# Kernel tuning notes

Hardware: AMD Instinct MI355X
Metric: run time of the kernel (lower is better)

## Reference

```python
import jax, jax.numpy as jnp
import numpy as np

N = 200_000   # nodes
E = 3_200_000 # edges (avg degree 16)
H = 64        # hidden_size == state_size
A = 2         # annotation_size


def _mlp(x, w1, b1, w2, b2, w3, b3):
    x = jax.nn.relu(x @ w1.T + b1)
    x = jax.nn.relu(x @ w2.T + b2)
    return x @ w3.T + b3


def setup_inputs() -> dict:
    key = jax.random.key(0)
    ks = jax.random.split(key, 24)
    s = 0.1
    d = {}
    d["x0"] = jax.random.normal(ks[0], (N, H - A), jnp.float32)
    d["annotations"] = jax.random.uniform(ks[1], (N, A), jnp.float32)
    d["edges"] = jax.random.randint(ks[2], (E, 2), 0, N, jnp.int32)
    d["eligible"] = jax.random.randint(ks[3], (4096,), 0, N, jnp.int32)
    d["W_msg"] = jax.random.normal(ks[4], (H, H), jnp.float32) * s
    d["b_msg"] = jnp.zeros((H,), jnp.float32)
    d["gru_Wih"] = jax.random.normal(ks[5], (3 * H, H), jnp.float32) * s
    d["gru_Whh"] = jax.random.normal(ks[6], (3 * H, H), jnp.float32) * s
    d["gru_bih"] = jnp.zeros((3 * H,), jnp.float32)
    d["gru_bhh"] = jnp.zeros((3 * H,), jnp.float32)
    # MLP heads: (prefix, out_dim)
    heads = [("sn", 1), ("st", 2), ("co", 128), ("sp", 100)]
    i = 7
    for p, od in heads:
        d[p + "_w1"] = jax.random.normal(ks[i], (64, H), jnp.float32) * s; i += 1
        d[p + "_b1"] = jnp.zeros((64,), jnp.float32)
        d[p + "_w2"] = jax.random.normal(ks[i], (64, 64), jnp.float32) * s; i += 1
        d[p + "_w2"] = d[p + "_w2"]
        d[p + "_b2"] = jnp.zeros((64,), jnp.float32)
        d[p + "_w3"] = jax.random.normal(ks[i], (od, 64), jnp.float32) * s; i += 1
        d[p + "_b3"] = jnp.zeros((od,), jnp.float32)
    return d


def _ggnn(x0, annotations, edges, W_msg, b_msg, gru_Wih, gru_Whh, gru_bih, gru_bhh):
    # initial node state: annotations appended, padded to hidden_size  -> [N, H]
    h = jnp.concatenate([x0, annotations], axis=-1)
    src, dst = edges[:, 0], edges[:, 1]
    # one edge type, one timestep (layer_timesteps=[1])
    m = h[src] @ W_msg.T + b_msg                       # [E, H] gather + tiny GEMM
    agg = jax.ops.segment_sum(m, dst, num_segments=h.shape[0])  # [N, H] scatter-add
    # torch.nn.GRUCell(agg, h); gate order: r, z, n
    gx = agg @ gru_Wih.T + gru_bih
    gh = h @ gru_Whh.T + gru_bhh
    xr, xz, xn = jnp.split(gx, 3, axis=-1)
    hr, hz, hn = jnp.split(gh, 3, axis=-1)
    r = jax.nn.sigmoid(xr + hr)
    z = jax.nn.sigmoid(xz + hz)
    n = jnp.tanh(xn + r * hn)
    return (1.0 - z) * n + z * h


def reference(x0, annotations, edges, eligible, W_msg, b_msg, gru_Wih, gru_Whh,
              gru_bih, gru_bhh, sn_w1, sn_b1, sn_w2, sn_b2, sn_w3, sn_b3,
              st_w1, st_b1, st_w2, st_b2, st_w3, st_b3,
              co_w1, co_b1, co_w2, co_b2, co_w3, co_b3,
              sp_w1, sp_b1, sp_w2, sp_b2, sp_w3, sp_b3):
    h = _ggnn(x0, annotations, edges, W_msg, b_msg, gru_Wih, gru_Whh, gru_bih, gru_bhh)
    select_out = _mlp(h, sn_w1, sn_b1, sn_w2, sn_b2, sn_w3, sn_b3)  # [N, 1]
    rel = jnp.argmax(select_out[eligible, 0])
    node_index = eligible[rel]
    h_node = h[node_index]                                           # [H]
    task_out = _mlp(h_node, st_w1, st_b1, st_w2, st_b2, st_w3, st_b3)   # [2]
    color_out = _mlp(h_node, co_w1, co_b1, co_w2, co_b2, co_w3, co_b3)  # [128]
    split_out = _mlp(h_node, sp_w1, sp_b1, sp_w2, sp_b2, sp_w3, sp_b3)  # [100]
    return (select_out, node_index, task_out, color_out, split_out)
```

## Files before the change

kernel.cpp:

```cpp
#include <hip/hip_runtime.h>

#define THREADS 256
#define CAP 10240

__device__ __forceinline__ float sigm_(float x) {
  return 1.0f / (1.0f + __expf(-x));
}
__device__ __forceinline__ float tanh_(float x) {
  float cx = fminf(15.0f, fmaxf(-15.0f, x));
  float a = __expf(2.0f * cx);
  return (a - 1.0f) / (a + 1.0f);
}

__global__ void k_build_h(const float* __restrict__ x0, const float* __restrict__ ann,
                          float* __restrict__ h, int N) {
  int t = blockIdx.x * THREADS + threadIdx.x;
  if (t >= N * 64) return;
  int v = t >> 6, c = t & 63;
  h[t] = (c < 62) ? x0[v * 62 + c] : ann[(v << 1) + (c - 62)];
}

__global__ void k_pre(const float* __restrict__ Wmsg, const float* __restrict__ bmsg,
                      const float* __restrict__ Wih, const float* __restrict__ Whh,
                      const float* __restrict__ sw1, const float* __restrict__ sw2,
                      float* __restrict__ Wct, float* __restrict__ Whht,
                      float* __restrict__ bmc, float* __restrict__ w1t, float* __restrict__ w2t) {
  int g = blockIdx.x * THREADS + threadIdx.x;
  int gs = gridDim.x * THREADS;
  for (int idx = g; idx < 64 * 192; idx += gs) {
    int k = idx / 192, r = idx - k * 192;
    float acc = 0.f;
    for (int c = 0; c < 64; ++c) acc = fmaf(Wih[r * 64 + c], Wmsg[c * 64 + k], acc);
    Wct[idx]  = acc;
    Whht[idx] = Whh[r * 64 + k];
  }
  for (int r = g; r < 192; r += gs) {
    float acc = 0.f;
    for (int c = 0; c < 64; ++c) acc = fmaf(Wih[r * 64 + c], bmsg[c], acc);
    bmc[r] = acc;
  }
  for (int idx = g; idx < 64 * 64; idx += gs) {
    int k = idx >> 6, r = idx & 63;
    w1t[idx] = sw1[r * 64 + k];
    w2t[idx] = sw2[r * 64 + k];
  }
}


__global__ __launch_bounds__(THREADS) void k_binA(const int* __restrict__ edges,
                                                  int* __restrict__ bincnt,
                                                  int* __restrict__ binbuf, int E, int nbins) {
  __shared__ int cnt[1024];
  __shared__ int gb[1024];
  int t = threadIdx.x;
  for (int i = t; i < nbins; i += THREADS) cnt[i] = 0;
  __syncthreads();
  long e0 = (long)blockIdx.x * 2048;
  int bins[8], packs[8], ranks[8];
#pragma unroll
  for (int j = 0; j < 8; ++j) {
    long e = e0 + j * THREADS + t;
    bins[j] = -1;
    if (e < E) {
      int2 ed = ((const int2*)edges)[e];
      bins[j] = ed.y >> 9;
      packs[j] = (ed.x << 9) | (ed.y & 511);
      ranks[j] = atomicAdd(&cnt[bins[j]], 1);
    }
  }
  __syncthreads();
  for (int i = t; i < nbins; i += THREADS) gb[i] = cnt[i] ? atomicAdd(&bincnt[i], cnt[i]) : 0;
  __syncthreads();
#pragma unroll
  for (int j = 0; j < 8; ++j)
    if (bins[j] >= 0) {
      int pos = gb[bins[j]] + ranks[j];
      if (pos < CAP) binbuf[(long)bins[j] * CAP + pos] = packs[j];
    }
}

__global__ void k_binscan(const int* __restrict__ bincnt, int* __restrict__ binoff,
                          int* __restrict__ row_off, int nbins, int E, int N) {
  __shared__ int sm[1024];
  int t = threadIdx.x;
  sm[t] = (t < nbins) ? bincnt[t] : 0;
  __syncthreads();
  for (int o = 1; o < 1024; o <<= 1) {
    int v = (t >= o) ? sm[t - o] : 0;
    __syncthreads();
    sm[t] += v;
    __syncthreads();
  }
  if (t < nbins) binoff[t] = (t == 0) ? 0 : sm[t - 1];
  if (t == 0) { binoff[nbins] = E; row_off[N] = E; }
}

__global__ __launch_bounds__(THREADS) void k_binB(const int* __restrict__ binoff,
                                                  const int* __restrict__ bincnt,
                                                  const int* __restrict__ binbuf,
                                                  int* __restrict__ csr,
                                                  int* __restrict__ deg,
                                                  int* __restrict__ row_off, int N) {
  __shared__ int cnt[512], off[512], cur[512], ps[THREADS];
  int b = blockIdx.x, t = threadIdx.x;
  int nodebase = b << 9;
  int nn = min(512, N - nodebase);
  int ebeg = binoff[b];
  int cntE = min(bincnt[b], CAP);
  const int* seg = binbuf + (long)b * CAP;
  for (int i = t; i < 512; i += THREADS) cnt[i] = 0;
  __syncthreads();
  for (int e = t; e < cntE; e += THREADS)
    atomicAdd(&cnt[seg[e] & 511], 1);
  __syncthreads();
  int a0 = cnt[2 * t], a1 = cnt[2 * t + 1];
  ps[t] = a0 + a1;
  __syncthreads();
  for (int o = 1; o < THREADS; o <<= 1) {
    int v = (t >= o) ? ps[t - o] : 0;
    __syncthreads();
    ps[t] += v;
    __syncthreads();
  }
  int excl = (t == 0) ? 0 : ps[t - 1];
  off[2 * t] = excl;          cur[2 * t] = excl;
  off[2 * t + 1] = excl + a0; cur[2 * t + 1] = excl + a0;
  __syncthreads();
  for (int l = t; l < nn; l += THREADS) {
    deg[nodebase + l] = cnt[l];
    row_off[nodebase + l] = ebeg + off[l];
  }
  for (int e = t; e < cntE; e += THREADS) {
    int p = seg[e];
    int slot = atomicAdd(&cur[p & 511], 1);
    csr[ebeg + slot] = p >> 9;
  }
}

__global__ __launch_bounds__(THREADS, 3) void k_gru_sel(
    const int* __restrict__ row_off, const int* __restrict__ csr,
    const float* __restrict__ h, float* __restrict__ hn,
    const float* __restrict__ Wct, const float* __restrict__ Whht,
    const float* __restrict__ bmc, const float* __restrict__ bih, const float* __restrict__ bhh,
    const int* __restrict__ deg,
    const float* __restrict__ w1t, const float* __restrict__ b1,
    const float* __restrict__ w2t, const float* __restrict__ b2,
    const float* __restrict__ w3, const float* __restrict__ b3,
    float* __restrict__ sel_out) {
  __shared__ float St[64][68];
  __shared__ float Ht[64][68];
  const int t = threadIdx.x;
  const long base = (long)blockIdx.x * (64 * 64);
  const int nodebase = blockIdx.x * 64;

#pragma unroll
  for (int j = 0; j < 4; ++j) {
    int f = t + THREADS * j;
    int n = f >> 4;
    int k0 = (f & 15) << 2;
    float4 hv = *(const float4*)(h + base + n * 64 + k0);
    Ht[k0 + 0][n] = hv.x; Ht[k0 + 1][n] = hv.y; Ht[k0 + 2][n] = hv.z; Ht[k0 + 3][n] = hv.w;
  }

  {
    const float SC = 1048576.0f;
    const float ISC = 1.0f / 1048576.0f;
    int vl = t >> 2;
    int c16 = (t & 3) << 4;
    int v = nodebase + vl;
    int beg = row_off[v], end = row_off[v + 1];
    int acc[16];
#pragma unroll
    for (int j = 0; j < 16; ++j) acc[j] = 0;
    for (int i = beg; i < end; ++i) {
      const float4* hp = (const float4*)(h + (long)csr[i] * 64 + c16);
      float4 a = hp[0], b = hp[1], c = hp[2], d = hp[3];
      acc[0]  += __float2int_rn(a.x * SC); acc[1]  += __float2int_rn(a.y * SC);
      acc[2]  += __float2int_rn(a.z * SC); acc[3]  += __float2int_rn(a.w * SC);
      acc[4]  += __float2int_rn(b.x * SC); acc[5]  += __float2int_rn(b.y * SC);
      acc[6]  += __float2int_rn(b.z * SC); acc[7]  += __float2int_rn(b.w * SC);
      acc[8]  += __float2int_rn(c.x * SC); acc[9]  += __float2int_rn(c.y * SC);
      acc[10] += __float2int_rn(c.z * SC); acc[11] += __float2int_rn(c.w * SC);
      acc[12] += __float2int_rn(d.x * SC); acc[13] += __float2int_rn(d.y * SC);
      acc[14] += __float2int_rn(d.z * SC); acc[15] += __float2int_rn(d.w * SC);
    }
#pragma unroll
    for (int j = 0; j < 16; ++j) St[c16 + j][vl] = (float)acc[j] * ISC;
  }
  __syncthreads();

  const int ng = t & 15, rg = t >> 4;
  const int n4 = ng << 2, c0 = rg << 2;

  float arz[2][4][4] = {};
  float axn[4][4] = {};
  float ahn[4][4] = {};

  for (int k = 0; k < 64; ++k) {
    const float4 s4 = *(const float4*)&St[k][n4];
    const float4 h4 = *(const float4*)&Ht[k][n4];
    const float sv[4] = {s4.x, s4.y, s4.z, s4.w};
    const float hv[4] = {h4.x, h4.y, h4.z, h4.w};
    const float* wxp = Wct + k * 192 + c0;
    const float* whp = Whht + k * 192 + c0;
#pragma unroll
    for (int sec = 0; sec < 2; ++sec) {
      const float4 wx = *(const float4*)(wxp + sec * 64);
      const float4 wh = *(const float4*)(whp + sec * 64);
      const float wxv[4] = {wx.x, wx.y, wx.z, wx.w};
      const float whv[4] = {wh.x, wh.y, wh.z, wh.w};
#pragma unroll
      for (int ci = 0; ci < 4; ++ci)
#pragma unroll
        for (int nj = 0; nj < 4; ++nj) {
          arz[sec][ci][nj] = fmaf(wxv[ci], sv[nj], arz[sec][ci][nj]);
          arz[sec][ci][nj] = fmaf(whv[ci], hv[nj], arz[sec][ci][nj]);
        }
    }
    {
      const float4 wx = *(const float4*)(wxp + 128);
      const float4 wh = *(const float4*)(whp + 128);
      const float wxv[4] = {wx.x, wx.y, wx.z, wx.w};
      const float whv[4] = {wh.x, wh.y, wh.z, wh.w};
#pragma unroll
      for (int ci = 0; ci < 4; ++ci)
#pragma unroll
        for (int nj = 0; nj < 4; ++nj) {
          axn[ci][nj] = fmaf(wxv[ci], sv[nj], axn[ci][nj]);
          ahn[ci][nj] = fmaf(whv[ci], hv[nj], ahn[ci][nj]);
        }
    }
  }

  float degf[4];
#pragma unroll
  for (int nj = 0; nj < 4; ++nj) degf[nj] = (float)deg[nodebase + n4 + nj];

  float res[4][4];
#pragma unroll
  for (int ci = 0; ci < 4; ++ci) {
    const int c = c0 + ci;
    const float br = bmc[c];       const float cr = bih[c] + bhh[c];
    const float bz = bmc[64 + c];  const float cz = bih[64 + c] + bhh[64 + c];
    const float bn = bmc[128 + c]; const float ci2 = bih[128 + c];
    const float ch = bhh[128 + c];
#pragma unroll
    for (int nj = 0; nj < 4; ++nj) {
      float r = sigm_(arz[0][ci][nj] + degf[nj] * br + cr);
      float z = sigm_(arz[1][ci][nj] + degf[nj] * bz + cz);
      float xn = axn[ci][nj] + degf[nj] * bn + ci2;
      float hnv = ahn[ci][nj] + ch;
      float nn = tanh_(fmaf(r, hnv, xn));
      float hold = Ht[c][n4 + nj];
      res[ci][nj] = fmaf(1.f - z, nn, z * hold);
    }
  }
#pragma unroll
  for (int nj = 0; nj < 4; ++nj) {
    float4 o = make_float4(res[0][nj], res[1][nj], res[2][nj], res[3][nj]);
    *(float4*)(hn + base + (n4 + nj) * 64 + c0) = o;
  }

  __syncthreads();
#pragma unroll
  for (int ci = 0; ci < 4; ++ci) {
    *(float4*)&St[c0 + ci][n4] = make_float4(res[ci][0], res[ci][1], res[ci][2], res[ci][3]);
  }
  __syncthreads();

  float acc[4][4] = {};
  for (int k = 0; k < 64; ++k) {
    const float4 a4 = *(const float4*)&St[k][n4];
    const float av[4] = {a4.x, a4.y, a4.z, a4.w};
    const float4 w4 = *(const float4*)(w1t + k * 64 + c0);
    const float wv[4] = {w4.x, w4.y, w4.z, w4.w};
#pragma unroll
    for (int ri = 0; ri < 4; ++ri)
#pragma unroll
      for (int nj = 0; nj < 4; ++nj)
        acc[ri][nj] = fmaf(wv[ri], av[nj], acc[ri][nj]);
  }
  __syncthreads();
#pragma unroll
  for (int ri = 0; ri < 4; ++ri) {
    const float bb = b1[c0 + ri];
    float4 o;
    o.x = fmaxf(acc[ri][0] + bb, 0.f);
    o.y = fmaxf(acc[ri][1] + bb, 0.f);
    o.z = fmaxf(acc[ri][2] + bb, 0.f);
    o.w = fmaxf(acc[ri][3] + bb, 0.f);
    *(float4*)&Ht[c0 + ri][n4] = o;
  }
  __syncthreads();

  float acc2[4][4] = {};
  for (int k = 0; k < 64; ++k) {
    const float4 a4 = *(const float4*)&Ht[k][n4];
    const float av[4] = {a4.x, a4.y, a4.z, a4.w};
    const float4 w4 = *(const float4*)(w2t + k * 64 + c0);
    const float wv[4] = {w4.x, w4.y, w4.z, w4.w};
#pragma unroll
    for (int ri = 0; ri < 4; ++ri)
#pragma unroll
      for (int nj = 0; nj < 4; ++nj)
        acc2[ri][nj] = fmaf(wv[ri], av[nj], acc2[ri][nj]);
  }
  __syncthreads();
#pragma unroll
  for (int ri = 0; ri < 4; ++ri) {
    const float bb = b2[c0 + ri];
    float4 o;
    o.x = fmaxf(acc2[ri][0] + bb, 0.f);
    o.y = fmaxf(acc2[ri][1] + bb, 0.f);
    o.z = fmaxf(acc2[ri][2] + bb, 0.f);
    o.w = fmaxf(acc2[ri][3] + bb, 0.f);
    *(float4*)&St[c0 + ri][n4] = o;
  }
  __syncthreads();

  if (t < 64) {
    float acc3 = b3[0];
    for (int k = 0; k < 64; ++k) acc3 = fmaf(St[k][t], w3[k], acc3);
    sel_out[nodebase + t] = acc3;
  }
}

__global__ void k_argmax(const float* __restrict__ sel, const int* __restrict__ elig,
                         int ne, float* __restrict__ out_idx, int* __restrict__ idx_ws) {
  __shared__ float bv[256];
  __shared__ int br[256];
  const int t = threadIdx.x;
  float best = -3.402823466e+38f;
  int brel = 0x7fffffff;
  for (int i = t; i < ne; i += 256) {
    float v = sel[elig[i]];
    if (v > best || (v == best && i < brel)) { best = v; brel = i; }
  }
  bv[t] = best; br[t] = brel;
  __syncthreads();
  for (int off = 128; off > 0; off >>= 1) {
    if (t < off) {
      float v2 = bv[t + off]; int r2 = br[t + off];
      if (v2 > bv[t] || (v2 == bv[t] && r2 < br[t])) { bv[t] = v2; br[t] = r2; }
    }
    __syncthreads();
  }
  if (t == 0) {
    int node = elig[br[0]];
    out_idx[0] = (float)node;
    idx_ws[0] = node;
  }
}

struct HeadP {
  const float *w1, *b1, *w2, *b2, *w3, *b3;
  int od, off;
};

__global__ void k_heads(const float* __restrict__ hnew, const int* __restrict__ idx_p,
                        HeadP p0, HeadP p1, HeadP p2, float* __restrict__ outF) {
  HeadP p = (blockIdx.x == 0) ? p0 : ((blockIdx.x == 1) ? p1 : p2);
  __shared__ float hh[64], a1[64], a2[64];
  const int t = threadIdx.x;
  const int node = idx_p[0];
  if (t < 64) hh[t] = hnew[(long)node * 64 + t];
  __syncthreads();
  if (t < 64) {
    float acc = p.b1[t];
    for (int k = 0; k < 64; ++k) acc = fmaf(p.w1[t * 64 + k], hh[k], acc);
    a1[t] = fmaxf(acc, 0.f);
  }
  __syncthreads();
  if (t < 64) {
    float acc = p.b2[t];
    for (int k = 0; k < 64; ++k) acc = fmaf(p.w2[t * 64 + k], a1[k], acc);
    a2[t] = fmaxf(acc, 0.f);
  }
  __syncthreads();
  for (int o = t; o < p.od; o += blockDim.x) {
    float acc = p.b3[o];
    for (int k = 0; k < 64; ++k) acc = fmaf(p.w3[o * 64 + k], a2[k], acc);
    outF[p.off + o] = acc;
  }
}

extern "C" void kernel_launch(void* const* d_in, const int* in_sizes, int n_in,
                              void* d_out, int out_size, void* d_ws, size_t ws_size,
                              hipStream_t stream) {
  const float* x0    = (const float*)d_in[0];
  const float* ann   = (const float*)d_in[1];
  const int*   edges = (const int*)d_in[2];
  const int*   elig  = (const int*)d_in[3];
  const float* Wmsg  = (const float*)d_in[4];
  const float* bmsg  = (const float*)d_in[5];
  const float* Wih   = (const float*)d_in[6];
  const float* Whh   = (const float*)d_in[7];
  const float* bih   = (const float*)d_in[8];
  const float* bhh   = (const float*)d_in[9];

  const int N  = in_sizes[0] / 62;
  const int E  = in_sizes[2] / 2;
  const int NE = in_sizes[3];
  const int NBINS = (N + 511) >> 9;

  float* ws = (float*)d_ws;
  size_t off = 0;
  float* hn      = ws + off; off += (size_t)N * 64;
  int*   deg     = (int*)(ws + off); off += N;
  float* h       = ws + off; off += (size_t)N * 64;
  float* Wct     = ws + off; off += 64 * 192;
  float* Whht    = ws + off; off += 64 * 192;
  float* bmc     = ws + off; off += 192;
  float* w1t     = ws + off; off += 64 * 64;
  float* w2t     = ws + off; off += 64 * 64;
  int*   idxp    = (int*)(ws + off); off += 1;
  int*   row_off = (int*)(ws + off); off += (size_t)N + 1;
  int*   bincnt  = (int*)(ws + off); off += 1024;
  int*   binoff  = (int*)(ws + off); off += 1025;
  int*   csr     = (int*)(ws + off); off += E;
  int*   binbuf  = (int*)hn;

  float* outF = (float*)d_out;

  hipMemsetAsync(bincnt, 0, 1024 * sizeof(int), stream);

  k_build_h<<<(N * 64 + THREADS - 1) / THREADS, THREADS, 0, stream>>>(x0, ann, h, N);
  k_pre<<<64, THREADS, 0, stream>>>(Wmsg, bmsg, Wih, Whh,
                                    (const float*)d_in[10], (const float*)d_in[12],
                                    Wct, Whht, bmc, w1t, w2t);

  const int EB = (E + 2047) / 2048;
  k_binA<<<EB, THREADS, 0, stream>>>(edges, bincnt, binbuf, E, NBINS);
  k_binscan<<<1, 1024, 0, stream>>>(bincnt, binoff, row_off, NBINS, E, N);
  k_binB<<<NBINS, THREADS, 0, stream>>>(binoff, bincnt, binbuf, csr, deg, row_off, N);

  k_gru_sel<<<N / 64, THREADS, 0, stream>>>(row_off, csr, h, hn,
                                            Wct, Whht, bmc, bih, bhh, deg,
                                            w1t, (const float*)d_in[11],
                                            w2t, (const float*)d_in[13],
                                            (const float*)d_in[14], (const float*)d_in[15],
                                            outF);
  k_argmax<<<1, 256, 0, stream>>>(outF, elig, NE, outF + N, idxp);

  HeadP p0 = {(const float*)d_in[16], (const float*)d_in[17], (const float*)d_in[18],
              (const float*)d_in[19], (const float*)d_in[20], (const float*)d_in[21],
              2, N + 1};
  HeadP p1 = {(const float*)d_in[22], (const float*)d_in[23], (const float*)d_in[24],
              (const float*)d_in[25], (const float*)d_in[26], (const float*)d_in[27],
              128, N + 3};
  HeadP p2 = {(const float*)d_in[28], (const float*)d_in[29], (const float*)d_in[30],
              (const float*)d_in[31], (const float*)d_in[32], (const float*)d_in[33],
              100, N + 131};
  k_heads<<<3, 128, 0, stream>>>(hn, idxp, p0, p1, p2, outF);
}
```

Baseline: 628.4 us.

## Drop CSR build; sort bin edges per block in LDS inside GRU kernel

Removes the binscan and binB kernels. Each GRU block now scans its 512-node bin buffer, keeps edges for its own 64 nodes, and builds a local CSR in shared memory, which it uses for the gather. It also fuses build_h with the weight precompute and argmax with the heads, which cuts launches. The trade-off is that each bin is read redundantly by eight blocks, plus more shared memory, and a risk of truncation if a 64-node group exceeds LCAP edges.

```diff
diff --git a/kernel.cpp b/kernel.cpp
--- a/kernel.cpp
+++ b/kernel.cpp
@@ -2,6 +2,7 @@
 
 #define THREADS 256
 #define CAP 10240
+#define LCAP 1408
 
 __device__ __forceinline__ float sigm_(float x) {
   return 1.0f / (1.0f + __expf(-x));
@@ -12,21 +13,23 @@
   return (a - 1.0f) / (a + 1.0f);
 }
 
-__global__ void k_build_h(const float* __restrict__ x0, const float* __restrict__ ann,
-                          float* __restrict__ h, int N) {
-  int t = blockIdx.x * THREADS + threadIdx.x;
-  if (t >= N * 64) return;
-  int v = t >> 6, c = t & 63;
-  h[t] = (c < 62) ? x0[v * 62 + c] : ann[(v << 1) + (c - 62)];
-}
-
-__global__ void k_pre(const float* __restrict__ Wmsg, const float* __restrict__ bmsg,
-                      const float* __restrict__ Wih, const float* __restrict__ Whh,
-                      const float* __restrict__ sw1, const float* __restrict__ sw2,
-                      float* __restrict__ Wct, float* __restrict__ Whht,
-                      float* __restrict__ bmc, float* __restrict__ w1t, float* __restrict__ w2t) {
-  int g = blockIdx.x * THREADS + threadIdx.x;
-  int gs = gridDim.x * THREADS;
+__global__ void k_init(const float* __restrict__ x0, const float* __restrict__ ann,
+                       float* __restrict__ h, int N, int NBH,
+                       const float* __restrict__ Wmsg, const float* __restrict__ bmsg,
+                       const float* __restrict__ Wih, const float* __restrict__ Whh,
+                       const float* __restrict__ sw1, const float* __restrict__ sw2,
+                       float* __restrict__ Wct, float* __restrict__ Whht,
+                       float* __restrict__ bmc, float* __restrict__ w1t,
+                       float* __restrict__ w2t) {
+  if (blockIdx.x < NBH) {
+    int t = blockIdx.x * THREADS + threadIdx.x;
+    if (t >= N * 64) return;
+    int v = t >> 6, c = t & 63;
+    h[t] = (c < 62) ? x0[v * 62 + c] : ann[(v << 1) + (c - 62)];
+    return;
+  }
+  int g = (blockIdx.x - NBH) * THREADS + threadIdx.x;
+  int gs = 64 * THREADS;
   for (int idx = g; idx < 64 * 192; idx += gs) {
     int k = idx / 192, r = idx - k * 192;
     float acc = 0.f;
@@ -45,7 +48,6 @@
     w2t[idx] = sw2[r * 64 + k];
   }
 }
-
 
 __global__ __launch_bounds__(THREADS) void k_binA(const int* __restrict__ edges,
                                                   int* __restrict__ bincnt,
@@ -79,79 +81,28 @@
     }
 }
 
-__global__ void k_binscan(const int* __restrict__ bincnt, int* __restrict__ binoff,
-                          int* __restrict__ row_off, int nbins, int E, int N) {
-  __shared__ int sm[1024];
-  int t = threadIdx.x;
-  sm[t] = (t < nbins) ? bincnt[t] : 0;
-  __syncthreads();
-  for (int o = 1; o < 1024; o <<= 1) {
-    int v = (t >= o) ? sm[t - o] : 0;
-    __syncthreads();
-    sm[t] += v;
-    __syncthreads();
-  }
-  if (t < nbins) binoff[t] = (t == 0) ? 0 : sm[t - 1];
-  if (t == 0) { binoff[nbins] = E; row_off[N] = E; }
-}
-
-__global__ __launch_bounds__(THREADS) void k_binB(const int* __restrict__ binoff,
-                                                  const int* __restrict__ bincnt,
-                                                  const int* __restrict__ binbuf,
-                                                  int* __restrict__ csr,
-                                                  int* __restrict__ deg,
-                                                  int* __restrict__ row_off, int N) {
-  __shared__ int cnt[512], off[512], cur[512], ps[THREADS];
-  int b = blockIdx.x, t = threadIdx.x;
-  int nodebase = b << 9;
-  int nn = min(512, N - nodebase);
-  int ebeg = binoff[b];
-  int cntE = min(bincnt[b], CAP);
-  const int* seg = binbuf + (long)b * CAP;
-  for (int i = t; i < 512; i += THREADS) cnt[i] = 0;
-  __syncthreads();
-  for (int e = t; e < cntE; e += THREADS)
-    atomicAdd(&cnt[seg[e] & 511], 1);
-  __syncthreads();
-  int a0 = cnt[2 * t], a1 = cnt[2 * t + 1];
-  ps[t] = a0 + a1;
-  __syncthreads();
-  for (int o = 1; o < THREADS; o <<= 1) {
-    int v = (t >= o) ? ps[t - o] : 0;
-    __syncthreads();
-    ps[t] += v;
-    __syncthreads();
-  }
-  int excl = (t == 0) ? 0 : ps[t - 1];
-  off[2 * t] = excl;          cur[2 * t] = excl;
-  off[2 * t + 1] = excl + a0; cur[2 * t + 1] = excl + a0;
-  __syncthreads();
-  for (int l = t; l < nn; l += THREADS) {
-    deg[nodebase + l] = cnt[l];
-    row_off[nodebase + l] = ebeg + off[l];
-  }
-  for (int e = t; e < cntE; e += THREADS) {
-    int p = seg[e];
-    int slot = atomicAdd(&cur[p & 511], 1);
-    csr[ebeg + slot] = p >> 9;
-  }
-}
-
 __global__ __launch_bounds__(THREADS, 3) void k_gru_sel(
-    const int* __restrict__ row_off, const int* __restrict__ csr,
+    const int* __restrict__ bincnt, const int* __restrict__ binbuf,
     const float* __restrict__ h, float* __restrict__ hn,
     const float* __restrict__ Wct, const float* __restrict__ Whht,
     const float* __restrict__ bmc, const float* __restrict__ bih, const float* __restrict__ bhh,
-    const int* __restrict__ deg,
     const float* __restrict__ w1t, const float* __restrict__ b1,
     const float* __restrict__ w2t, const float* __restrict__ b2,
     const float* __restrict__ w3, const float* __restrict__ b3,
     float* __restrict__ sel_out) {
   __shared__ float St[64][68];
   __shared__ float Ht[64][68];
+  __shared__ int elist[LCAP];
+  __shared__ int ecnt[64], eoff[64], ecur[64];
   const int t = threadIdx.x;
   const long base = (long)blockIdx.x * (64 * 64);
   const int nodebase = blockIdx.x * 64;
+  const int b512 = blockIdx.x >> 3;
+  const int sub = blockIdx.x & 7;
+  const int segn = min(bincnt[b512], CAP);
+  const int* seg = binbuf + (long)b512 * CAP;
+
+  if (t < 64) ecnt[t] = 0;
 
 #pragma unroll
   for (int j = 0; j < 4; ++j) {
@@ -161,19 +112,68 @@
     float4 hv = *(const float4*)(h + base + n * 64 + k0);
     Ht[k0 + 0][n] = hv.x; Ht[k0 + 1][n] = hv.y; Ht[k0 + 2][n] = hv.z; Ht[k0 + 3][n] = hv.w;
   }
+  __syncthreads();
+
+  for (int i = t; i < segn; i += THREADS) {
+    int p = seg[i];
+    if (((p >> 6) & 7) == sub) atomicAdd(&ecnt[p & 63], 1);
+  }
+  __syncthreads();
+  if (t < 64) eoff[t] = ecnt[t];
+  __syncthreads();
+  for (int o = 1; o < 64; o <<= 1) {
+    int v = (t >= o && t < 64) ? eoff[t - o] : 0;
+    __syncthreads();
+    if (t < 64) eoff[t] += v;
+    __syncthreads();
+  }
+  if (t < 64) { int ex = eoff[t] - ecnt[t]; eoff[t] = ex; ecur[t] = ex; }
+  __syncthreads();
+  for (int i = t; i < segn; i += THREADS) {
+    int p = seg[i];
+    if (((p >> 6) & 7) == sub) {
+      int slot = atomicAdd(&ecur[p & 63], 1);
+      if (slot < LCAP) elist[slot] = p >> 9;
+    }
+  }
+  __syncthreads();
 
   {
     const float SC = 1048576.0f;
     const float ISC = 1.0f / 1048576.0f;
     int vl = t >> 2;
     int c16 = (t & 3) << 4;
-    int v = nodebase + vl;
-    int beg = row_off[v], end = row_off[v + 1];
+    int beg = eoff[vl];
+    int num = min(ecnt[vl], LCAP - beg);
+    if (num < 0) num = 0;
     int acc[16];
 #pragma unroll
     for (int j = 0; j < 16; ++j) acc[j] = 0;
-    for (int i = beg; i < end; ++i) {
-      const float4* hp = (const float4*)(h + (long)csr[i] * 64 + c16);
+    int i = 0;
+    for (; i + 1 < num; i += 2) {
+      const float4* hp0 = (const float4*)(h + (long)elist[beg + i] * 64 + c16);
+      const float4* hp1 = (const float4*)(h + (long)elist[beg + i + 1] * 64 + c16);
+      float4 a0 = hp0[0], b0 = hp0[1], c0_ = hp0[2], d0 = hp0[3];
+      float4 a1 = hp1[0], b1_ = hp1[1], c1 = hp1[2], d1 = hp1[3];
+      acc[0]  += __float2int_rn(a0.x * SC) + __float2int_rn(a1.x * SC);
+      acc[1]  += __float2int_rn(a0.y * SC) + __float2int_rn(a1.y * SC);
+      acc[2]  += __float2int_rn(a0.z * SC) + __float2int_rn(a1.z * SC);
+      acc[3]  += __float2int_rn(a0.w * SC) + __float2int_rn(a1.w * SC);
+      acc[4]  += __float2int_rn(b0.x * SC) + __float2int_rn(b1_.x * SC);
+      acc[5]  += __float2int_rn(b0.y * SC) + __float2int_rn(b1_.y * SC);
+      acc[6]  += __float2int_rn(b0.z * SC) + __float2int_rn(b1_.z * SC);
+      acc[7]  += __float2int_rn(b0.w * SC) + __float2int_rn(b1_.w * SC);
+      acc[8]  += __float2int_rn(c0_.x * SC) + __float2int_rn(c1.x * SC);
+      acc[9]  += __float2int_rn(c0_.y * SC) + __float2int_rn(c1.y * SC);
+      acc[10] += __float2int_rn(c0_.z * SC) + __float2int_rn(c1.z * SC);
+      acc[11] += __float2int_rn(c0_.w * SC) + __float2int_rn(c1.w * SC);
+      acc[12] += __float2int_rn(d0.x * SC) + __float2int_rn(d1.x * SC);
+      acc[13] += __float2int_rn(d0.y * SC) + __float2int_rn(d1.y * SC);
+      acc[14] += __float2int_rn(d0.z * SC) + __float2int_rn(d1.z * SC);
+      acc[15] += __float2int_rn(d0.w * SC) + __float2int_rn(d1.w * SC);
+    }
+    if (i < num) {
+      const float4* hp = (const float4*)(h + (long)elist[beg + i] * 64 + c16);
       float4 a = hp[0], b = hp[1], c = hp[2], d = hp[3];
       acc[0]  += __float2int_rn(a.x * SC); acc[1]  += __float2int_rn(a.y * SC);
       acc[2]  += __float2int_rn(a.z * SC); acc[3]  += __float2int_rn(a.w * SC);
@@ -234,7 +234,7 @@
 
   float degf[4];
 #pragma unroll
-  for (int nj = 0; nj < 4; ++nj) degf[nj] = (float)deg[nodebase + n4 + nj];
+  for (int nj = 0; nj < 4; ++nj) degf[nj] = (float)ecnt[n4 + nj];
 
   float res[4][4];
 #pragma unroll
@@ -325,10 +325,18 @@
   }
 }
 
-__global__ void k_argmax(const float* __restrict__ sel, const int* __restrict__ elig,
-                         int ne, float* __restrict__ out_idx, int* __restrict__ idx_ws) {
+struct HeadP {
+  const float *w1, *b1, *w2, *b2, *w3, *b3;
+  int od, off;
+};
+
+__global__ void k_argmax_heads(const float* __restrict__ sel, const int* __restrict__ elig,
+                               int ne, const float* __restrict__ hnew,
+                               HeadP p0, HeadP p1, HeadP p2,
+                               float* __restrict__ outF, int N) {
   __shared__ float bv[256];
   __shared__ int br[256];
+  __shared__ float hh[64], a1[64], a2[64];
   const int t = threadIdx.x;
   float best = -3.402823466e+38f;
   int brel = 0x7fffffff;
@@ -347,40 +355,34 @@
   }
   if (t == 0) {
     int node = elig[br[0]];
-    out_idx[0] = (float)node;
-    idx_ws[0] = node;
-  }
-}
-
-struct HeadP {
-  const float *w1, *b1, *w2, *b2, *w3, *b3;
-  int od, off;
-};
-
-__global__ void k_heads(const float* __restrict__ hnew, const int* __restrict__ idx_p,
-                        HeadP p0, HeadP p1, HeadP p2, float* __restrict__ outF) {
-  HeadP p = (blockIdx.x == 0) ? p0 : ((blockIdx.x == 1) ? p1 : p2);
-  __shared__ float hh[64], a1[64], a2[64];
-  const int t = threadIdx.x;
-  const int node = idx_p[0];
+    outF[N] = (float)node;
+    br[0] = node;
+  }
+  __syncthreads();
+  const int node = br[0];
   if (t < 64) hh[t] = hnew[(long)node * 64 + t];
   __syncthreads();
-  if (t < 64) {
-    float acc = p.b1[t];
-    for (int k = 0; k < 64; ++k) acc = fmaf(p.w1[t * 64 + k], hh[k], acc);
-    a1[t] = fmaxf(acc, 0.f);
-  }
-  __syncthreads();
-  if (t < 64) {
-    float acc = p.b2[t];
-    for (int k = 0; k < 64; ++k) acc = fmaf(p.w2[t * 64 + k], a1[k], acc);
-    a2[t] = fmaxf(acc, 0.f);
-  }
-  __syncthreads();
-  for (int o = t; o < p.od; o += blockDim.x) {
-    float acc = p.b3[o];
-    for (int k = 0; k < 64; ++k) acc = fmaf(p.w3[o * 64 + k], a2[k], acc);
-    outF[p.off + o] = acc;
+
+  for (int hsel = 0; hsel < 3; ++hsel) {
+    HeadP p = (hsel == 0) ? p0 : ((hsel == 1) ? p1 : p2);
+    if (t < 64) {
+      float acc = p.b1[t];
+      for (int k = 0; k < 64; ++k) acc = fmaf(p.w1[t * 64 + k], hh[k], acc);
+      a1[t] = fmaxf(acc, 0.f);
+    }
+    __syncthreads();
+    if (t < 64) {
+      float acc = p.b2[t];
+      for (int k = 0; k < 64; ++k) acc = fmaf(p.w2[t * 64 + k], a1[k], acc);
+      a2[t] = fmaxf(acc, 0.f);
+    }
+    __syncthreads();
+    for (int o = t; o < p.od; o += 256) {
+      float acc = p.b3[o];
+      for (int k = 0; k < 64; ++k) acc = fmaf(p.w3[o * 64 + k], a2[k], acc);
+      outF[p.off + o] = acc;
+    }
+    __syncthreads();
   }
 }
 
@@ -406,41 +408,34 @@
   float* ws = (float*)d_ws;
   size_t off = 0;
   float* hn      = ws + off; off += (size_t)N * 64;
-  int*   deg     = (int*)(ws + off); off += N;
   float* h       = ws + off; off += (size_t)N * 64;
   float* Wct     = ws + off; off += 64 * 192;
   float* Whht    = ws + off; off += 64 * 192;
   float* bmc     = ws + off; off += 192;
   float* w1t     = ws + off; off += 64 * 64;
   float* w2t     = ws + off; off += 64 * 64;
-  int*   idxp    = (int*)(ws + off); off += 1;
-  int*   row_off = (int*)(ws + off); off += (size_t)N + 1;
   int*   bincnt  = (int*)(ws + off); off += 1024;
-  int*   binoff  = (int*)(ws + off); off += 1025;
-  int*   csr     = (int*)(ws + off); off += E;
-  int*   binbuf  = (int*)hn;
+  int*   binbuf  = (int*)(ws + off); off += (size_t)NBINS * CAP;
 
   float* outF = (float*)d_out;
 
   hipMemsetAsync(bincnt, 0, 1024 * sizeof(int), stream);
 
-  k_build_h<<<(N * 64 + THREADS - 1) / THREADS, THREADS, 0, stream>>>(x0, ann, h, N);
-  k_pre<<<64, THREADS, 0, stream>>>(Wmsg, bmsg, Wih, Whh,
-                                    (const float*)d_in[10], (const float*)d_in[12],
-                                    Wct, Whht, bmc, w1t, w2t);
+  const int NBH = (N * 64 + THREADS - 1) / THREADS;
+  k_init<<<NBH + 64, THREADS, 0, stream>>>(x0, ann, h, N, NBH,
+                                           Wmsg, bmsg, Wih, Whh,
+                                           (const float*)d_in[10], (const float*)d_in[12],
+                                           Wct, Whht, bmc, w1t, w2t);
 
   const int EB = (E + 2047) / 2048;
   k_binA<<<EB, THREADS, 0, stream>>>(edges, bincnt, binbuf, E, NBINS);
-  k_binscan<<<1, 1024, 0, stream>>>(bincnt, binoff, row_off, NBINS, E, N);
-  k_binB<<<NBINS, THREADS, 0, stream>>>(binoff, bincnt, binbuf, csr, deg, row_off, N);
-
-  k_gru_sel<<<N / 64, THREADS, 0, stream>>>(row_off, csr, h, hn,
-                                            Wct, Whht, bmc, bih, bhh, deg,
+
+  k_gru_sel<<<N / 64, THREADS, 0, stream>>>(bincnt, binbuf, h, hn,
+                                            Wct, Whht, bmc, bih, bhh,
                                             w1t, (const float*)d_in[11],
                                             w2t, (const float*)d_in[13],
                                             (const float*)d_in[14], (const float*)d_in[15],
                                             outF);
-  k_argmax<<<1, 256, 0, stream>>>(outF, elig, NE, outF + N, idxp);
 
   HeadP p0 = {(const float*)d_in[16], (const float*)d_in[17], (const float*)d_in[18],
               (const float*)d_in[19], (const float*)d_in[20], (const float*)d_in[21],
@@ -451,5 +446,5 @@
   HeadP p2 = {(const float*)d_in[28], (const float*)d_in[29], (const float*)d_in[30],
               (const float*)d_in[31], (const float*)d_in[32], (const float*)d_in[33],
               100, N + 131};
-  k_heads<<<3, 128, 0, stream>>>(hn, idxp, p0, p1, p2, outF);
-}
+  k_argmax_heads<<<1, 256, 0, stream>>>(outF, elig, NE, hn, p0, p1, p2, outF, N);
+}
```

Result: slower. 646.1 us (+2.8%).
